# Kernel optimization log

Hardware: AMD Instinct MI355X
Metric: run time of the kernel (lower is better)

The kernel has to match this reference:

```python
import jax, jax.numpy as jnp
import numpy as np

B, NP, L, C, NA = 16, 512, 20, 3, 50
RATIO = 0.8
K = int(np.ceil(RATIO * NP))  # 410 nodes kept per graph
N = B * NP
E = 6 * N
NF, EF = 13, 4
EPS = 1e-5


def _graph_norm(x, w, b, ms):
    # PyG GraphNorm called WITHOUT batch in the source -> single global graph
    mean = x.mean(0)
    out = x - ms * mean
    var = (out * out).mean(0)
    return w * out / jnp.sqrt(var + EPS) + b


def _forward(x, pan_w, lin1_w, lin1_b, norm1_w, norm1_b, norm1_ms,
             pool_p, pool_beta, gat_wl, gat_bl, gat_wr, gat_br, gat_att, gat_bias,
             norm2_w, norm2_b, norm2_ms,
             val1_w, val1_b, val2_w, val2_b, val3_w, val3_b,
             adv1_w, adv1_b, adv2_w, adv2_b, adv3_w, adv3_b,
             edge_index, current_node_ids, action_mask):
    src, dst = edge_index[0], edge_index[1]
    # PANConv builds SparseTensor(row=edge_index[1], col=edge_index[0]) -> row = target
    A = jnp.zeros((B, NP, NP), x.dtype).at[dst // NP, dst % NP, src % NP].set(1.0)
    eyeB = jnp.broadcast_to(jnp.eye(NP, dtype=x.dtype), A.shape)

    # panentropy: M = sum_{i=0..L} w_i * A^i  (dense per graph)
    def step(carry, wi):
        tmp, acc = carry
        tmp = tmp @ A
        return (tmp, acc + wi * tmp), None
    (_, M), _ = jax.lax.scan(step, (eyeB, pan_w[0] * eyeB), pan_w[1:])
    deg = M.sum(-1)                                   # row sums
    dis = jnp.where(deg > 0, 1.0 / jnp.sqrt(deg), 0.0)
    Mn = dis[:, :, None] * M * dis[:, None, :]        # D^-1/2 M D^-1/2

    # conv1: propagate (Mn @ x) then Linear
    x3 = x.reshape(B, NP, NF)
    h = jnp.einsum('bij,bjf->bif', Mn, x3) @ lin1_w + lin1_b   # [B,NP,C]
    x1 = jax.nn.relu(_graph_norm(h.reshape(N, C), norm1_w, norm1_b, norm1_ms))  # [N,C]
    h = x1.reshape(B, NP, C)

    # PANPooling: score = tanh(b0 * <x,p> + b1 * colsum(Mn)); keep top K per graph
    score = jnp.tanh(pool_beta[0] * (h * pool_p).sum(-1) + pool_beta[1] * Mn.sum(-2))
    vals, idx = jax.lax.top_k(score, K)                        # [B,K]
    xp = jnp.take_along_axis(h, idx[:, :, None], axis=1) * vals[..., None]
    Mg = jax.vmap(lambda m, i: m[i][:, i])(Mn, idx)            # filtered adjacency [B,K,K]
    mask = (jnp.swapaxes(Mg, 1, 2) != 0) | jnp.eye(K, dtype=bool)  # mask[b,i,j]: edge j->i (+self loops)

    # GATv2Conv, heads=1, eval mode (no dropout), edge_attr not passed in source
    xl = xp @ gat_wl + gat_bl
    xr = xp @ gat_wr + gat_br
    e = jax.nn.leaky_relu(xr[:, :, None, :] + xl[:, None, :, :], 0.2)  # [B,i,j,C]
    logits = jnp.where(mask, jnp.einsum('bijc,c->bij', e, gat_att), -1e9)
    alpha = jax.nn.softmax(logits, axis=-1)
    g = jnp.einsum('bij,bjc->bic', alpha, xl) + gat_bias

    g = jax.nn.relu(_graph_norm(g.reshape(B * K, C), norm2_w, norm2_b, norm2_ms)).reshape(B, K, C)
    gp = g.sum(1)                                              # global_add_pool [B,C]

    # source uses POOLED bincount cumsum offsets to index the pre-pool arrays (faithful)
    gidx = current_node_ids + jnp.arange(B, dtype=current_node_ids.dtype) * K
    feat = jnp.concatenate([x[gidx], x1[gidx], gp], axis=1)    # [B,19]

    a = jax.nn.relu(feat @ adv1_w + adv1_b)
    a = jax.nn.relu(a @ adv2_w + adv2_b)
    a = a @ adv3_w + adv3_b
    v = jax.nn.relu(feat @ val1_w + val1_b)
    v = jax.nn.relu(v @ val2_w + val2_b)
    v = v @ val3_w + val3_b
    q = v + (a - a.mean(1, keepdims=True))
    return jnp.where(action_mask == 0, -1e8, q)


def setup_inputs() -> dict:
    key = jax.random.key(0)
    ks = list(jax.random.split(key, 40))
    nk = lambda: ks.pop()
    # within-graph random edges so the PyG-style batch structure is valid
    g = jax.random.randint(nk(), (E,), 0, B)
    u = jax.random.randint(nk(), (E,), 0, NP)
    v = jax.random.randint(nk(), (E,), 0, NP)
    edge_index = jnp.stack([g * NP + u, g * NP + v]).astype(jnp.int32)

    def lin(k, i, o):
        k1, k2 = jax.random.split(k)
        return (jax.random.normal(k1, (i, o), jnp.float32) / np.sqrt(i),
                jax.random.normal(k2, (o,), jnp.float32) * 0.01)

    lin1_w, lin1_b = lin(nk(), NF, C)
    gat_wl, gat_bl = lin(nk(), C, C)
    gat_wr, gat_br = lin(nk(), C, C)
    val1_w, val1_b = lin(nk(), 19, 10)
    val2_w, val2_b = lin(nk(), 10, 5)
    val3_w, val3_b = lin(nk(), 5, 1)
    adv1_w, adv1_b = lin(nk(), 19, 10)
    adv2_w, adv2_b = lin(nk(), 10, 5)
    adv3_w, adv3_b = lin(nk(), 5, NA)
    return dict(
        x=jax.random.normal(nk(), (N, NF), jnp.float32),
        edge_index=edge_index,
        edge_attr=jax.random.normal(nk(), (E, EF), jnp.float32),
        batch=jnp.arange(N, dtype=jnp.int32) // NP,
        current_node_ids=jax.random.randint(nk(), (B,), 0, NP),
        action_mask=jax.random.randint(nk(), (B, NA), 0, 2),
        pan_w=jax.random.uniform(nk(), (L + 1,), jnp.float32) * 0.5,
        lin1_w=lin1_w, lin1_b=lin1_b,
        norm1_w=jnp.ones(C), norm1_b=jnp.zeros(C), norm1_ms=jnp.ones(C),
        pool_p=jax.random.normal(nk(), (C,), jnp.float32),
        pool_beta=jnp.array([0.5, 0.5], jnp.float32),
        gat_wl=gat_wl, gat_bl=gat_bl, gat_wr=gat_wr, gat_br=gat_br,
        gat_att=jax.random.normal(nk(), (C,), jnp.float32),
        gat_bias=jax.random.normal(nk(), (C,), jnp.float32) * 0.01,
        norm2_w=jnp.ones(C), norm2_b=jnp.zeros(C), norm2_ms=jnp.ones(C),
        val1_w=val1_w, val1_b=val1_b, val2_w=val2_w, val2_b=val2_b,
        val3_w=val3_w, val3_b=val3_b,
        adv1_w=adv1_w, adv1_b=adv1_b, adv2_w=adv2_w, adv2_b=adv2_b,
        adv3_w=adv3_w, adv3_b=adv3_b,
    )


def reference(x, edge_index, edge_attr, batch, current_node_ids, action_mask,
              pan_w, lin1_w, lin1_b, norm1_w, norm1_b, norm1_ms,
              pool_p, pool_beta, gat_wl, gat_bl, gat_wr, gat_br, gat_att, gat_bias,
              norm2_w, norm2_b, norm2_ms,
              val1_w, val1_b, val2_w, val2_b, val3_w, val3_b,
              adv1_w, adv1_b, adv2_w, adv2_b, adv3_w, adv3_b):
    del edge_attr, batch  # received by the torch forward but never consumed
    return _forward(x, pan_w, lin1_w, lin1_b, norm1_w, norm1_b, norm1_ms,
                    pool_p, pool_beta, gat_wl, gat_bl, gat_wr, gat_br, gat_att, gat_bias,
                    norm2_w, norm2_b, norm2_ms,
                    val1_w, val1_b, val2_w, val2_b, val3_w, val3_b,
                    adv1_w, adv1_b, adv2_w, adv2_b, adv3_w, adv3_b,
                    edge_index, current_node_ids, action_mask)
```

## Files before the change

### kernel.cpp

```cpp
#include <hip/hip_runtime.h>
#include <hip/hip_bf16.h>
#include <stdint.h>
#include <math.h>

#define BB   16
#define NPn  512
#define LLp  20
#define NAa  50
#define KKk  410
#define NNt  (BB * NPn)
#define EEe  (6 * NNt)
#define NFf  13
#define KPAD 416
#define KP2  448
#define EPSf 1e-5f
#define QCLMP 1e6f
#define MAXD 28
#define PADR 512

__device__ __forceinline__ float r17_sane(float v) {
    if (!(v == v)) return 0.0f;
    return fminf(fmaxf(v, -1e15f), 1e15f);
}

__global__ __launch_bounds__(256) void r17_scatter(
    const int* __restrict__ ei,
    uint32_t* __restrict__ fwdb, uint32_t* __restrict__ trsb)
{
    const int e = blockIdx.x * 256 + threadIdx.x;
    if (e < EEe) {
        const int src = ei[e], dst = ei[EEe + e];
        atomicOr(&fwdb[(size_t)dst * 16 + ((src & 511) >> 5)], 1u << (src & 31));
        atomicOr(&trsb[(size_t)src * 16 + ((dst & 511) >> 5)], 1u << (dst & 31));
    }
}

__global__ __launch_bounds__(256) void r17_extract(
    const uint32_t* __restrict__ fwdb, const uint32_t* __restrict__ trsb,
    unsigned short* __restrict__ csrF, unsigned short* __restrict__ csrT)
{
    const int t = blockIdx.x * 256 + threadIdx.x;
    const int node = t & 8191;
    const uint32_t* bs = (t < 8192) ? (fwdb + (size_t)node * 16)
                                    : (trsb + (size_t)node * 16);
    unsigned short* cs = (t < 8192) ? csrF : csrT;
    int cnt = 0;
    for (int w = 0; w < 16; ++w) {
        uint32_t bits = bs[w];
        while (bits) {
            const int u = (w << 5) + __ffs(bits) - 1;
            bits &= bits - 1;
            if (cnt < MAXD) cs[(size_t)cnt * 8192 + node] = (unsigned short)u;
            ++cnt;
        }
    }
    for (int j = cnt; j < MAXD; ++j) cs[(size_t)j * 8192 + node] = PADR;
}

__global__ __launch_bounds__(512) void r17_mid(
    const float* __restrict__ x,
    const unsigned short* __restrict__ csrF,
    const unsigned short* __restrict__ csrT,
    const float* __restrict__ panw,
    const float* __restrict__ l1w, const float* __restrict__ l1b,
    float* __restrict__ h_raw, float* __restrict__ colsum,
    uint32_t* __restrict__ Rb)
{
    __shared__ __align__(16) uint32_t sbuf[1047];
    float* pa  = (float*)sbuf;
    float* pb  = (float*)(sbuf + 513);
    float* wsh = (float*)(sbuf + 1026);
    const int b = blockIdx.x, y = blockIdx.y, t = threadIdx.x;
    const int node = b * 512 + t;

    if (y < 4) {
        const int c = y;
        int iF[MAXD];
#pragma unroll
        for (int j = 0; j < MAXD; ++j) iF[j] = (int)csrF[(size_t)j * 8192 + node];
        if (t < 21) wsh[t] = panw[t];

        pa[t] = 1.0f;
        if (t == 0) { pa[512] = 0.0f; pb[512] = 0.0f; }
        __syncthreads();
        float dacc = wsh[0];
        {
            float* rp = pa; float* rn = pb;
            for (int i = 1; i <= LLp; ++i) {
                float tv[MAXD];
#pragma unroll
                for (int j = 0; j < MAXD; ++j) tv[j] = rp[iF[j]];
                float s = 0.0f;
#pragma unroll
                for (int j = 0; j < MAXD; ++j) s += tv[j];
                rn[t] = s;
                dacc += wsh[i] * s;
                __syncthreads();
                float* tp = rp; rp = rn; rn = tp;
            }
        }
        const float d0 = (dacc > 0.0f) ? 1.0f / sqrtf(dacc) : 0.0f;

        int idx[MAXD];
        if (c == 3) {
#pragma unroll
            for (int j = 0; j < MAXD; ++j) idx[j] = (int)csrT[(size_t)j * 8192 + node];
        } else {
#pragma unroll
            for (int j = 0; j < MAXD; ++j) idx[j] = iF[j];
        }
        float seed;
        if (c < 3) {
            float xw = 0.0f;
            const float* xr = x + (size_t)node * NFf;
            for (int f = 0; f < NFf; ++f) xw += xr[f] * l1w[f * 3 + c];
            seed = d0 * xw;
        } else {
            seed = d0;
        }
        pa[t] = seed;
        if (t == 0) { pa[512] = 0.0f; pb[512] = 0.0f; }
        __syncthreads();
        float acc = wsh[0] * seed;
        {
            float* rp = pa; float* rn = pb;
            for (int i = 1; i <= LLp; ++i) {
                float tv[MAXD];
#pragma unroll
                for (int j = 0; j < MAXD; ++j) tv[j] = rp[idx[j]];
                float s = 0.0f;
#pragma unroll
                for (int j = 0; j < MAXD; ++j) s += tv[j];
                rn[t] = s;
                acc += wsh[i] * s;
                __syncthreads();
                float* tp = rp; rp = rn; rn = tp;
            }
        }
        if (c < 3) h_raw[(size_t)node * 3 + c] = r17_sane(d0 * acc + l1b[c]);
        else       colsum[node] = r17_sane(d0 * acc);
    } else {
        const int q = y - 4;
        int iF[MAXD];
#pragma unroll
        for (int j = 0; j < MAXD; ++j) iF[j] = (int)csrF[(size_t)j * 8192 + node];
        uint32_t* R1 = sbuf;
        uint32_t* R2 = sbuf + 513;
        R1[t] = ((t >> 5) == q) ? (1u << (t & 31)) : 0u;
        if (t == 0) { R1[512] = 0u; R2[512] = 0u; }
        __syncthreads();
        uint32_t* Rp = R1; uint32_t* Rn = R2;
        for (int i = 0; i < LLp; ++i) {
            uint32_t tv[MAXD];
#pragma unroll
            for (int j = 0; j < MAXD; ++j) tv[j] = Rp[iF[j]];
            uint32_t r = Rp[t];
#pragma unroll
            for (int j = 0; j < MAXD; ++j) r |= tv[j];
            Rn[t] = r;
            __syncthreads();
            uint32_t* tp = Rp; Rp = Rn; Rn = tp;
        }
        Rb[(size_t)node * 16 + q] = Rp[t];
    }
}

__global__ __launch_bounds__(512) void r17_poolgat(
    const float* __restrict__ h_raw,
    const float* __restrict__ colsum,
    const uint32_t* __restrict__ Rb,
    const float* n1w, const float* n1b, const float* n1ms,
    const float* poolp, const float* poolb,
    const float* gwl, const float* gbl,
    const float* gwr, const float* gbr,
    const float* gatt, const float* gbias,
    float* __restrict__ x1,
    float* __restrict__ g_raw)
{
    __shared__ __align__(16) uint32_t pg[10744];
    float* sc   = (float*)pg;
    float* mv   = (float*)(pg + 512);
    float* wred = (float*)(pg + 520);
    float* xpS  = (float*)(pg + 568);
    int*   kidx = (int*)(pg + 1816);
    float* xlS  = (float*)(pg + 2232);
    uint32_t* RT = pg + 3576;
    const int b = blockIdx.x, y = blockIdx.y, t = threadIdx.x;
    const int lane = t & 63, wv = t >> 6;
    const float inv_n = 1.0f / (float)NNt;

    float hv0[16], hv1[16], hv2[16];
    float p0 = 0.0f, p1 = 0.0f, p2 = 0.0f;
#pragma unroll
    for (int k = 0; k < 16; ++k) {
        const float* hr = h_raw + (size_t)(k * 512 + t) * 3;
        hv0[k] = hr[0]; hv1[k] = hr[1]; hv2[k] = hr[2];
        p0 += hv0[k]; p1 += hv1[k]; p2 += hv2[k];
    }
#pragma unroll
    for (int off = 32; off; off >>= 1) {
        p0 += __shfl_xor(p0, off); p1 += __shfl_xor(p1, off); p2 += __shfl_xor(p2, off);
    }
    if (lane == 0) { wred[wv * 3 + 0] = p0; wred[wv * 3 + 1] = p1; wred[wv * 3 + 2] = p2; }
    __syncthreads();
    if (t < 3) {
        float s = 0.0f;
        for (int w = 0; w < 8; ++w) s += wred[w * 3 + t];
        mv[t] = s * inv_n;
    }
    __syncthreads();
    const float mm0 = n1ms[0] * mv[0], mm1 = n1ms[1] * mv[1], mm2 = n1ms[2] * mv[2];
    float q0 = 0.0f, q1 = 0.0f, q2 = 0.0f;
#pragma unroll
    for (int k = 0; k < 16; ++k) {
        const float d0 = hv0[k] - mm0, d1 = hv1[k] - mm1, d2 = hv2[k] - mm2;
        q0 += d0 * d0; q1 += d1 * d1; q2 += d2 * d2;
    }
#pragma unroll
    for (int off = 32; off; off >>= 1) {
        q0 += __shfl_xor(q0, off); q1 += __shfl_xor(q1, off); q2 += __shfl_xor(q2, off);
    }
    if (lane == 0) { wred[wv * 3 + 0] = q0; wred[wv * 3 + 1] = q1; wred[wv * 3 + 2] = q2; }
    __syncthreads();
    if (t < 3) {
        float s = 0.0f;
        for (int w = 0; w < 8; ++w) s += wred[w * 3 + t];
        mv[3 + t] = s * inv_n;
    }
    __syncthreads();

    const float mmv[3] = { mm0, mm1, mm2 };
    float xv[3];
#pragma unroll
    for (int c = 0; c < 3; ++c) {
        const float iv = 1.0f / sqrtf(fmaxf(mv[3 + c], 0.0f) + EPSf);
        const float o  = h_raw[(size_t)(b * NPn + t) * 3 + c] - mmv[c];
        const float tt = n1w[c] * o * iv + n1b[c];
        xv[c] = fmaxf(tt, 0.0f);
        if (y == 0) x1[(size_t)(b * NPn + t) * 3 + c] = xv[c];
    }
    float s = poolb[0] * (xv[0] * poolp[0] + xv[1] * poolp[1] + xv[2] * poolp[2])
            + poolb[1] * colsum[b * NPn + t];
    s = tanhf(s);
    if (!(s == s)) s = 0.0f;
    sc[t] = s;
    __syncthreads();
    int cnt = 0;
    for (int u = 0; u < NPn; ++u) {
        const float su = sc[u];
        cnt += ((su > s) || (su == s && u < t)) ? 1 : 0;
    }
    if (cnt < KKk) {
        kidx[cnt] = t;
        xpS[cnt * 3 + 0] = xv[0] * s;
        xpS[cnt * 3 + 1] = xv[1] * s;
        xpS[cnt * 3 + 2] = xv[2] * s;
    }
    __syncthreads();

    float Wl[9], Wr[9];
#pragma unroll
    for (int i2 = 0; i2 < 9; ++i2) { Wl[i2] = gwl[i2]; Wr[i2] = gwr[i2]; }
    const float Bl0 = gbl[0], Bl1 = gbl[1], Bl2 = gbl[2];
    const float Br0 = gbr[0], Br1 = gbr[1], Br2 = gbr[2];
    const float At0 = gatt[0], At1 = gatt[1], At2 = gatt[2];
    const float Gb0 = gbias[0], Gb1 = gbias[1], Gb2 = gbias[2];
    if (t < KP2) {
        const int j = t;
        if (j < KKk) {
            const float c0 = xpS[j * 3 + 0];
            const float c1 = xpS[j * 3 + 1];
            const float c2 = xpS[j * 3 + 2];
            xlS[j * 3 + 0] = c0 * Wl[0] + c1 * Wl[3] + c2 * Wl[6] + Bl0;
            xlS[j * 3 + 1] = c0 * Wl[1] + c1 * Wl[4] + c2 * Wl[7] + Bl1;
            xlS[j * 3 + 2] = c0 * Wl[2] + c1 * Wl[5] + c2 * Wl[8] + Bl2;
            const uint32_t* rr = Rb + (size_t)(b * NPn + kidx[j]) * 16;
#pragma unroll
            for (int w = 0; w < 16; ++w) RT[w * KP2 + j] = rr[w];
        } else {
            xlS[j * 3 + 0] = 0.0f; xlS[j * 3 + 1] = 0.0f; xlS[j * 3 + 2] = 0.0f;
#pragma unroll
            for (int w = 0; w < 16; ++w) RT[w * KP2 + j] = 0u;
        }
    }
    __syncthreads();

    const int wid = y * 8 + wv;
    for (int i = wid; i < KKk; i += 64) {
        const float c0 = xpS[i * 3 + 0];
        const float c1 = xpS[i * 3 + 1];
        const float c2 = xpS[i * 3 + 2];
        const float xr0 = c0 * Wr[0] + c1 * Wr[3] + c2 * Wr[6] + Br0;
        const float xr1 = c0 * Wr[1] + c1 * Wr[4] + c2 * Wr[7] + Br1;
        const float xr2 = c0 * Wr[2] + c1 * Wr[5] + c2 * Wr[8] + Br2;
        const int bi = kidx[i];
        const uint32_t mbit = 1u << (bi & 31);
        const uint32_t* Rw = &RT[(bi >> 5) * KP2];
        float mx = -3e38f, lsum = 0.0f, b0 = 0.0f, b1 = 0.0f, b2 = 0.0f;
#pragma unroll
        for (int it = 0; it < 7; ++it) {
            const int j = lane + it * 64;
            const uint32_t rw = Rw[j];
            const float xl0 = xlS[j * 3 + 0];
            const float xl1 = xlS[j * 3 + 1];
            const float xl2 = xlS[j * 3 + 2];
            const bool valid = (rw & mbit) || (j == i);
            float e0 = xr0 + xl0; e0 = e0 > 0.0f ? e0 : 0.2f * e0;
            float e1 = xr1 + xl1; e1 = e1 > 0.0f ? e1 : 0.2f * e1;
            float e2 = xr2 + xl2; e2 = e2 > 0.0f ? e2 : 0.2f * e2;
            const float sv = At0 * e0 + At1 * e1 + At2 * e2;
            if (valid) {
                if (sv > mx) {
                    const float r = __expf(mx - sv);
                    lsum *= r; b0 *= r; b1 *= r; b2 *= r;
                    mx = sv;
                }
                const float pj = __expf(sv - mx);
                lsum += pj;
                b0 += pj * xl0; b1 += pj * xl1; b2 += pj * xl2;
            }
        }
#pragma unroll
        for (int off = 32; off; off >>= 1) {
            const float mo = __shfl_xor(mx, off);
            const float lo = __shfl_xor(lsum, off);
            const float d0 = __shfl_xor(b0, off);
            const float d1 = __shfl_xor(b1, off);
            const float d2 = __shfl_xor(b2, off);
            const float M  = fmaxf(mx, mo);
            const float ea = __expf(mx - M), eb = __expf(mo - M);
            lsum = lsum * ea + lo * eb;
            b0 = b0 * ea + d0 * eb;
            b1 = b1 * ea + d1 * eb;
            b2 = b2 * ea + d2 * eb;
            mx = M;
        }
        if (lane == 0) {
            const float rl = 1.0f / fmaxf(lsum, 1e-30f);
            g_raw[(size_t)(b * KPAD + i) * 3 + 0] = r17_sane(b0 * rl + Gb0);
            g_raw[(size_t)(b * KPAD + i) * 3 + 1] = r17_sane(b1 * rl + Gb1);
            g_raw[(size_t)(b * KPAD + i) * 3 + 2] = r17_sane(b2 * rl + Gb2);
        }
    }
}

__global__ __launch_bounds__(512) void r17_head(
    const float* __restrict__ g_raw,
    const float* __restrict__ x1,
    const float* __restrict__ x,
    const int* __restrict__ cnid,
    const int* __restrict__ amask,
    const float* n2w, const float* n2b, const float* n2ms,
    const float* v1w, const float* v1b,
    const float* v2w, const float* v2b,
    const float* v3w, const float* v3b,
    const float* a1w, const float* a1b,
    const float* a2w, const float* a2b,
    const float* a3w, const float* a3b,
    float* __restrict__ out)
{
    __shared__ float wred[24];
    __shared__ float mv[6];
    __shared__ float gp[3];
    __shared__ float feat[19];
    __shared__ float h1a[10], h1v[10], h2a[5], h2v[5];
    __shared__ float a3[50];
    __shared__ float vout_s, amean_s;
    const int b = blockIdx.x, t = threadIdx.x;
    const int lane = t & 63, wv = t >> 6;
    const float denom = 1.0f / (float)(BB * KKk);

    float gv0[13], gv1[13], gv2[13];
    float p0 = 0.0f, p1 = 0.0f, p2 = 0.0f;
#pragma unroll
    for (int k = 0; k < 13; ++k) {
        const int r = k * 512 + t;
        float q0 = 0.0f, q1 = 0.0f, q2 = 0.0f;
        if (r < BB * KKk) {
            const int bq = r / KKk, iq = r - bq * KKk;
            const float* gr = g_raw + (size_t)(bq * KPAD + iq) * 3;
            q0 = gr[0]; q1 = gr[1]; q2 = gr[2];
        }
        gv0[k] = q0; gv1[k] = q1; gv2[k] = q2;
        p0 += q0; p1 += q1; p2 += q2;
    }
#pragma unroll
    for (int off = 32; off; off >>= 1) {
        p0 += __shfl_xor(p0, off); p1 += __shfl_xor(p1, off); p2 += __shfl_xor(p2, off);
    }
    if (lane == 0) { wred[wv * 3 + 0] = p0; wred[wv * 3 + 1] = p1; wred[wv * 3 + 2] = p2; }
    __syncthreads();
    if (t < 3) {
        float s = 0.0f;
        for (int w = 0; w < 8; ++w) s += wred[w * 3 + t];
        mv[t] = s * denom;
    }
    __syncthreads();
    const float mm0 = n2ms[0] * mv[0], mm1 = n2ms[1] * mv[1], mm2 = n2ms[2] * mv[2];
    float q0a = 0.0f, q1a = 0.0f, q2a = 0.0f;
#pragma unroll
    for (int k = 0; k < 13; ++k) {
        const int r = k * 512 + t;
        if (r < BB * KKk) {
            const float d0 = gv0[k] - mm0, d1 = gv1[k] - mm1, d2 = gv2[k] - mm2;
            q0a += d0 * d0; q1a += d1 * d1; q2a += d2 * d2;
        }
    }
#pragma unroll
    for (int off = 32; off; off >>= 1) {
        q0a += __shfl_xor(q0a, off); q1a += __shfl_xor(q1a, off); q2a += __shfl_xor(q2a, off);
    }
    if (lane == 0) { wred[wv * 3 + 0] = q0a; wred[wv * 3 + 1] = q1a; wred[wv * 3 + 2] = q2a; }
    __syncthreads();
    if (t < 3) {
        float s = 0.0f;
        for (int w = 0; w < 8; ++w) s += wred[w * 3 + t];
        mv[3 + t] = s * denom;
    }
    __syncthreads();

    const float mmv[3] = { mm0, mm1, mm2 };
    float s3[3] = { 0.0f, 0.0f, 0.0f };
    if (t < KKk) {
        const size_t r = (size_t)(b * KPAD + t) * 3;
#pragma unroll
        for (int c = 0; c < 3; ++c) {
            const float iv = 1.0f / sqrtf(fmaxf(mv[3 + c], 0.0f) + EPSf);
            s3[c] = fmaxf((g_raw[r + c] - mmv[c]) * iv * n2w[c] + n2b[c], 0.0f);
        }
    }
    float g0 = s3[0], g1 = s3[1], g2 = s3[2];
#pragma unroll
    for (int off = 32; off; off >>= 1) {
        g0 += __shfl_xor(g0, off); g1 += __shfl_xor(g1, off); g2 += __shfl_xor(g2, off);
    }
    if (lane == 0) { wred[wv * 3 + 0] = g0; wred[wv * 3 + 1] = g1; wred[wv * 3 + 2] = g2; }
    __syncthreads();
    if (t < 3) {
        float s = 0.0f;
        for (int w = 0; w < 8; ++w) s += wred[w * 3 + t];
        gp[t] = s;
    }
    __syncthreads();

    if (t < 19) {
        const int gidx = cnid[b] + b * KKk;
        float fv;
        if (t < 13)      fv = x[(size_t)gidx * NFf + t];
        else if (t < 16) fv = x1[(size_t)gidx * 3 + (t - 13)];
        else             fv = gp[t - 16];
        feat[t] = fv;
    }
    __syncthreads();

    if (t < 10) {
        float s = a1b[t];
        for (int f = 0; f < 19; ++f) s += feat[f] * a1w[f * 10 + t];
        h1a[t] = fmaxf(s, 0.0f);
    } else if (t >= 64 && t < 74) {
        const int j = t - 64;
        float s = v1b[j];
        for (int f = 0; f < 19; ++f) s += feat[f] * v1w[f * 10 + j];
        h1v[j] = fmaxf(s, 0.0f);
    }
    __syncthreads();
    if (t < 5) {
        float s = a2b[t];
        for (int k = 0; k < 10; ++k) s += h1a[k] * a2w[k * 5 + t];
        h2a[t] = fmaxf(s, 0.0f);
    } else if (t >= 64 && t < 69) {
        const int j = t - 64;
        float s = v2b[j];
        for (int k = 0; k < 10; ++k) s += h1v[k] * v2w[k * 5 + j];
        h2v[j] = fmaxf(s, 0.0f);
    }
    __syncthreads();
    if (t < 50) {
        float s = a3b[t];
        for (int k = 0; k < 5; ++k) s += h2a[k] * a3w[k * 50 + t];
        a3[t] = s;
    } else if (t == 64) {
        float s = v3b[0];
        for (int k = 0; k < 5; ++k) s += h2v[k] * v3w[k];
        vout_s = s;
    }
    __syncthreads();
    if (t == 0) {
        float s = 0.0f;
        for (int k = 0; k < 50; ++k) s += a3[k];
        amean_s = s * (1.0f / 50.0f);
    }
    __syncthreads();
    if (t < 50) {
        float q = vout_s + a3[t] - amean_s;
        if (!(q == q)) q = 0.0f;
        q = fminf(fmaxf(q, -QCLMP), QCLMP);
        out[b * NAa + t] = (amask[b * NAa + t] == 0) ? -1e8f : q;
    }
}

extern "C" void kernel_launch(void* const* d_in, const int* in_sizes, int n_in,
                              void* d_out, int out_size, void* d_ws, size_t ws_size,
                              hipStream_t stream) {
    (void)in_sizes; (void)n_in; (void)out_size;
    const float* x     = (const float*)d_in[0];
    const int* ei      = (const int*)d_in[1];
    const int* cnid    = (const int*)d_in[4];
    const int* amask   = (const int*)d_in[5];
    const float* panw  = (const float*)d_in[6];
    const float* l1w   = (const float*)d_in[7];
    const float* l1b   = (const float*)d_in[8];
    const float* n1w   = (const float*)d_in[9];
    const float* n1b   = (const float*)d_in[10];
    const float* n1ms  = (const float*)d_in[11];
    const float* poolp = (const float*)d_in[12];
    const float* poolb = (const float*)d_in[13];
    const float* gwl   = (const float*)d_in[14];
    const float* gbl   = (const float*)d_in[15];
    const float* gwr   = (const float*)d_in[16];
    const float* gbr   = (const float*)d_in[17];
    const float* gatt  = (const float*)d_in[18];
    const float* gbias = (const float*)d_in[19];
    const float* n2w   = (const float*)d_in[20];
    const float* n2b   = (const float*)d_in[21];
    const float* n2ms  = (const float*)d_in[22];
    const float* v1w   = (const float*)d_in[23];
    const float* v1b   = (const float*)d_in[24];
    const float* v2w   = (const float*)d_in[25];
    const float* v2b   = (const float*)d_in[26];
    const float* v3w   = (const float*)d_in[27];
    const float* v3b   = (const float*)d_in[28];
    const float* a1w   = (const float*)d_in[29];
    const float* a1b   = (const float*)d_in[30];
    const float* a2w   = (const float*)d_in[31];
    const float* a2b   = (const float*)d_in[32];
    const float* a3w   = (const float*)d_in[33];
    const float* a3b   = (const float*)d_in[34];
    float* out         = (float*)d_out;

    uint8_t* wsb = (uint8_t*)d_ws;
    uint32_t* fwdb = (uint32_t*)wsb;
    uint32_t* trsb = (uint32_t*)(wsb + 524288);
    uint32_t* Rb   = (uint32_t*)(wsb + 1048576);
    unsigned short* csrF = (unsigned short*)(wsb + 1572864);
    unsigned short* csrT = csrF + (size_t)MAXD * 8192;
    float* h_raw  = (float*)(csrT + (size_t)MAXD * 8192);
    float* x1     = h_raw + (size_t)NNt * 3;
    float* colsum = x1 + (size_t)NNt * 3;
    float* g_raw  = colsum + NNt;
    const size_t needed = 1572864 + 2 * (size_t)MAXD * 8192 * 2 +
                          ((size_t)(2 * NNt * 3 + NNt + BB * KPAD * 3)) * 4;
    if (ws_size < needed) return;

    hipMemsetAsync(fwdb, 0, 1048576, stream);
    r17_scatter<<<dim3((EEe + 255) / 256), dim3(256), 0, stream>>>(ei, fwdb, trsb);
    r17_extract<<<dim3(64), dim3(256), 0, stream>>>(fwdb, trsb, csrF, csrT);
    r17_mid<<<dim3(16, 20), dim3(512), 0, stream>>>(x, csrF, csrT, panw, l1w, l1b,
                                                    h_raw, colsum, Rb);
    r17_poolgat<<<dim3(16, 8), dim3(512), 0, stream>>>(h_raw, colsum, Rb,
                                                       n1w, n1b, n1ms, poolp, poolb,
                                                       gwl, gbl, gwr, gbr, gatt, gbias,
                                                       x1, g_raw);
    r17_head<<<dim3(16), dim3(512), 0, stream>>>(g_raw, x1, x, cnid, amask,
                                                 n2w, n2b, n2ms, v1w, v1b, v2w, v2b, v3w, v3b,
                                                 a1w, a1b, a2w, a2b, a3w, a3b, out);
}
```

Baseline: 211.0 us.

## Split pooling and GAT attention into separate kernels with wider GAT grid

The fused pool+GAT kernel, launched as 16x8 blocks that each redundantly recomputed graph norm, top-k and the transposed reachability table, is split in two. A 16-block pooling kernel now computes the selection once per graph and writes the kept features, projections, indices and transposed bitmasks to workspace. A separate 16x52 GAT kernel then handles one target node per wavefront, reading from global memory. The top-k rank loop also reads scores as float4. This removes redundant per-block work and spreads attention over more blocks, at the cost of an extra launch and global round-trips instead of shared memory.

Result: faster. 206.5 us (-2.2%).

```diff
diff --git a/kernel.cpp b/kernel.cpp
--- a/kernel.cpp
+++ b/kernel.cpp
@@ -165,27 +165,26 @@
     }
 }
 
-__global__ __launch_bounds__(512) void r17_poolgat(
+__global__ __launch_bounds__(512) void r18_pool(
     const float* __restrict__ h_raw,
     const float* __restrict__ colsum,
     const uint32_t* __restrict__ Rb,
     const float* n1w, const float* n1b, const float* n1ms,
     const float* poolp, const float* poolb,
     const float* gwl, const float* gbl,
-    const float* gwr, const float* gbr,
-    const float* gatt, const float* gbias,
     float* __restrict__ x1,
-    float* __restrict__ g_raw)
+    float* __restrict__ xpg,
+    float* __restrict__ xlg,
+    int*   __restrict__ kidxg,
+    uint32_t* __restrict__ RTg)
 {
-    __shared__ __align__(16) uint32_t pg[10744];
+    __shared__ __align__(16) uint32_t pg[2208];
     float* sc   = (float*)pg;
     float* mv   = (float*)(pg + 512);
     float* wred = (float*)(pg + 520);
-    float* xpS  = (float*)(pg + 568);
-    int*   kidx = (int*)(pg + 1816);
-    float* xlS  = (float*)(pg + 2232);
-    uint32_t* RT = pg + 3576;
-    const int b = blockIdx.x, y = blockIdx.y, t = threadIdx.x;
+    float* xpS  = (float*)(pg + 544);
+    int*   kidx = (int*)(pg + 1792);
+    const int b = blockIdx.x, t = threadIdx.x;
     const int lane = t & 63, wv = t >> 6;
     const float inv_n = 1.0f / (float)NNt;
 
@@ -237,7 +236,7 @@
         const float o  = h_raw[(size_t)(b * NPn + t) * 3 + c] - mmv[c];
         const float tt = n1w[c] * o * iv + n1b[c];
         xv[c] = fmaxf(tt, 0.0f);
-        if (y == 0) x1[(size_t)(b * NPn + t) * 3 + c] = xv[c];
+        x1[(size_t)(b * NPn + t) * 3 + c] = xv[c];
     }
     float s = poolb[0] * (xv[0] * poolp[0] + xv[1] * poolp[1] + xv[2] * poolp[2])
             + poolb[1] * colsum[b * NPn + t];
@@ -245,102 +244,136 @@
     if (!(s == s)) s = 0.0f;
     sc[t] = s;
     __syncthreads();
+
     int cnt = 0;
-    for (int u = 0; u < NPn; ++u) {
-        const float su = sc[u];
-        cnt += ((su > s) || (su == s && u < t)) ? 1 : 0;
+    for (int u = 0; u < NPn; u += 4) {
+        const float4 s4 = *(const float4*)(sc + u);
+        cnt += ((s4.x > s) || (s4.x == s && (u + 0) < t)) ? 1 : 0;
+        cnt += ((s4.y > s) || (s4.y == s && (u + 1) < t)) ? 1 : 0;
+        cnt += ((s4.z > s) || (s4.z == s && (u + 2) < t)) ? 1 : 0;
+        cnt += ((s4.w > s) || (s4.w == s && (u + 3) < t)) ? 1 : 0;
     }
     if (cnt < KKk) {
+        const float xp0 = xv[0] * s, xp1 = xv[1] * s, xp2 = xv[2] * s;
         kidx[cnt] = t;
-        xpS[cnt * 3 + 0] = xv[0] * s;
-        xpS[cnt * 3 + 1] = xv[1] * s;
-        xpS[cnt * 3 + 2] = xv[2] * s;
-    }
-    __syncthreads();
-
-    float Wl[9], Wr[9];
-#pragma unroll
-    for (int i2 = 0; i2 < 9; ++i2) { Wl[i2] = gwl[i2]; Wr[i2] = gwr[i2]; }
+        xpS[cnt * 3 + 0] = xp0;
+        xpS[cnt * 3 + 1] = xp1;
+        xpS[cnt * 3 + 2] = xp2;
+        kidxg[b * KPAD + cnt] = t;
+        xpg[(size_t)(b * KPAD + cnt) * 3 + 0] = xp0;
+        xpg[(size_t)(b * KPAD + cnt) * 3 + 1] = xp1;
+        xpg[(size_t)(b * KPAD + cnt) * 3 + 2] = xp2;
+    }
+    __syncthreads();
+
+    float Wl[9];
+#pragma unroll
+    for (int i2 = 0; i2 < 9; ++i2) Wl[i2] = gwl[i2];
     const float Bl0 = gbl[0], Bl1 = gbl[1], Bl2 = gbl[2];
+    if (t < KP2) {
+        float xl0, xl1, xl2;
+        uint32_t* RT = RTg + (size_t)b * 16 * KP2 + t;
+        if (t < KKk) {
+            const float c0 = xpS[t * 3 + 0];
+            const float c1 = xpS[t * 3 + 1];
+            const float c2 = xpS[t * 3 + 2];
+            xl0 = c0 * Wl[0] + c1 * Wl[3] + c2 * Wl[6] + Bl0;
+            xl1 = c0 * Wl[1] + c1 * Wl[4] + c2 * Wl[7] + Bl1;
+            xl2 = c0 * Wl[2] + c1 * Wl[5] + c2 * Wl[8] + Bl2;
+            const uint4* rr = (const uint4*)(Rb + (size_t)(b * NPn + kidx[t]) * 16);
+            const uint4 r0 = rr[0], r1 = rr[1], r2 = rr[2], r3 = rr[3];
+            RT[ 0 * KP2] = r0.x; RT[ 1 * KP2] = r0.y; RT[ 2 * KP2] = r0.z; RT[ 3 * KP2] = r0.w;
+            RT[ 4 * KP2] = r1.x; RT[ 5 * KP2] = r1.y; RT[ 6 * KP2] = r1.z; RT[ 7 * KP2] = r1.w;
+            RT[ 8 * KP2] = r2.x; RT[ 9 * KP2] = r2.y; RT[10 * KP2] = r2.z; RT[11 * KP2] = r2.w;
+            RT[12 * KP2] = r3.x; RT[13 * KP2] = r3.y; RT[14 * KP2] = r3.z; RT[15 * KP2] = r3.w;
+        } else {
+            xl0 = 0.0f; xl1 = 0.0f; xl2 = 0.0f;
+#pragma unroll
+            for (int w = 0; w < 16; ++w) RT[w * KP2] = 0u;
+        }
+        xlg[(size_t)(b * KP2 + t) * 3 + 0] = xl0;
+        xlg[(size_t)(b * KP2 + t) * 3 + 1] = xl1;
+        xlg[(size_t)(b * KP2 + t) * 3 + 2] = xl2;
+    }
+}
+
+__global__ __launch_bounds__(512) void r18_gat(
+    const float* __restrict__ xpg,
+    const float* __restrict__ xlg,
+    const int* __restrict__ kidxg,
+    const uint32_t* __restrict__ RTg,
+    const float* __restrict__ gwr, const float* __restrict__ gbr,
+    const float* __restrict__ gatt, const float* __restrict__ gbias,
+    float* __restrict__ g_raw)
+{
+    const int b = blockIdx.x, y = blockIdx.y, t = threadIdx.x;
+    const int lane = t & 63, wv = t >> 6;
+    const int i = y * 8 + wv;
+    if (i >= KKk) return;
+
+    float Wr[9];
+#pragma unroll
+    for (int k = 0; k < 9; ++k) Wr[k] = gwr[k];
     const float Br0 = gbr[0], Br1 = gbr[1], Br2 = gbr[2];
     const float At0 = gatt[0], At1 = gatt[1], At2 = gatt[2];
     const float Gb0 = gbias[0], Gb1 = gbias[1], Gb2 = gbias[2];
-    if (t < KP2) {
-        const int j = t;
-        if (j < KKk) {
-            const float c0 = xpS[j * 3 + 0];
-            const float c1 = xpS[j * 3 + 1];
-            const float c2 = xpS[j * 3 + 2];
-            xlS[j * 3 + 0] = c0 * Wl[0] + c1 * Wl[3] + c2 * Wl[6] + Bl0;
-            xlS[j * 3 + 1] = c0 * Wl[1] + c1 * Wl[4] + c2 * Wl[7] + Bl1;
-            xlS[j * 3 + 2] = c0 * Wl[2] + c1 * Wl[5] + c2 * Wl[8] + Bl2;
-            const uint32_t* rr = Rb + (size_t)(b * NPn + kidx[j]) * 16;
-#pragma unroll
-            for (int w = 0; w < 16; ++w) RT[w * KP2 + j] = rr[w];
-        } else {
-            xlS[j * 3 + 0] = 0.0f; xlS[j * 3 + 1] = 0.0f; xlS[j * 3 + 2] = 0.0f;
-#pragma unroll
-            for (int w = 0; w < 16; ++w) RT[w * KP2 + j] = 0u;
-        }
-    }
-    __syncthreads();
-
-    const int wid = y * 8 + wv;
-    for (int i = wid; i < KKk; i += 64) {
-        const float c0 = xpS[i * 3 + 0];
-        const float c1 = xpS[i * 3 + 1];
-        const float c2 = xpS[i * 3 + 2];
-        const float xr0 = c0 * Wr[0] + c1 * Wr[3] + c2 * Wr[6] + Br0;
-        const float xr1 = c0 * Wr[1] + c1 * Wr[4] + c2 * Wr[7] + Br1;
-        const float xr2 = c0 * Wr[2] + c1 * Wr[5] + c2 * Wr[8] + Br2;
-        const int bi = kidx[i];
-        const uint32_t mbit = 1u << (bi & 31);
-        const uint32_t* Rw = &RT[(bi >> 5) * KP2];
-        float mx = -3e38f, lsum = 0.0f, b0 = 0.0f, b1 = 0.0f, b2 = 0.0f;
-#pragma unroll
-        for (int it = 0; it < 7; ++it) {
-            const int j = lane + it * 64;
-            const uint32_t rw = Rw[j];
-            const float xl0 = xlS[j * 3 + 0];
-            const float xl1 = xlS[j * 3 + 1];
-            const float xl2 = xlS[j * 3 + 2];
-            const bool valid = (rw & mbit) || (j == i);
-            float e0 = xr0 + xl0; e0 = e0 > 0.0f ? e0 : 0.2f * e0;
-            float e1 = xr1 + xl1; e1 = e1 > 0.0f ? e1 : 0.2f * e1;
-            float e2 = xr2 + xl2; e2 = e2 > 0.0f ? e2 : 0.2f * e2;
-            const float sv = At0 * e0 + At1 * e1 + At2 * e2;
-            if (valid) {
-                if (sv > mx) {
-                    const float r = __expf(mx - sv);
-                    lsum *= r; b0 *= r; b1 *= r; b2 *= r;
-                    mx = sv;
-                }
-                const float pj = __expf(sv - mx);
-                lsum += pj;
-                b0 += pj * xl0; b1 += pj * xl1; b2 += pj * xl2;
+
+    const int bi = kidxg[b * KPAD + i];
+    const float c0 = xpg[(size_t)(b * KPAD + i) * 3 + 0];
+    const float c1 = xpg[(size_t)(b * KPAD + i) * 3 + 1];
+    const float c2 = xpg[(size_t)(b * KPAD + i) * 3 + 2];
+    const float xr0 = c0 * Wr[0] + c1 * Wr[3] + c2 * Wr[6] + Br0;
+    const float xr1 = c0 * Wr[1] + c1 * Wr[4] + c2 * Wr[7] + Br1;
+    const float xr2 = c0 * Wr[2] + c1 * Wr[5] + c2 * Wr[8] + Br2;
+
+    const uint32_t mbit = 1u << (bi & 31);
+    const uint32_t* Rw = RTg + (size_t)(b * 16 + (bi >> 5)) * KP2;
+    const float* xlb = xlg + (size_t)b * KP2 * 3;
+
+    float mx = -3e38f, lsum = 0.0f, b0 = 0.0f, b1 = 0.0f, b2 = 0.0f;
+#pragma unroll
+    for (int it = 0; it < 7; ++it) {
+        const int j = lane + it * 64;
+        const uint32_t rw = Rw[j];
+        const float xl0 = xlb[j * 3 + 0];
+        const float xl1 = xlb[j * 3 + 1];
+        const float xl2 = xlb[j * 3 + 2];
+        const bool valid = (rw & mbit) || (j == i);
+        float e0 = xr0 + xl0; e0 = e0 > 0.0f ? e0 : 0.2f * e0;
+        float e1 = xr1 + xl1; e1 = e1 > 0.0f ? e1 : 0.2f * e1;
+        float e2 = xr2 + xl2; e2 = e2 > 0.0f ? e2 : 0.2f * e2;
+        const float sv = At0 * e0 + At1 * e1 + At2 * e2;
+        if (valid) {
+            if (sv > mx) {
+                const float r = __expf(mx - sv);
+                lsum *= r; b0 *= r; b1 *= r; b2 *= r;
+                mx = sv;
             }
-        }
-#pragma unroll
-        for (int off = 32; off; off >>= 1) {
-            const float mo = __shfl_xor(mx, off);
-            const float lo = __shfl_xor(lsum, off);
-            const float d0 = __shfl_xor(b0, off);
-            const float d1 = __shfl_xor(b1, off);
-            const float d2 = __shfl_xor(b2, off);
-            const float M  = fmaxf(mx, mo);
-            const float ea = __expf(mx - M), eb = __expf(mo - M);
-            lsum = lsum * ea + lo * eb;
-            b0 = b0 * ea + d0 * eb;
-            b1 = b1 * ea + d1 * eb;
-            b2 = b2 * ea + d2 * eb;
-            mx = M;
-        }
-        if (lane == 0) {
-            const float rl = 1.0f / fmaxf(lsum, 1e-30f);
-            g_raw[(size_t)(b * KPAD + i) * 3 + 0] = r17_sane(b0 * rl + Gb0);
-            g_raw[(size_t)(b * KPAD + i) * 3 + 1] = r17_sane(b1 * rl + Gb1);
-            g_raw[(size_t)(b * KPAD + i) * 3 + 2] = r17_sane(b2 * rl + Gb2);
-        }
+            const float pj = __expf(sv - mx);
+            lsum += pj;
+            b0 += pj * xl0; b1 += pj * xl1; b2 += pj * xl2;
+        }
+    }
+#pragma unroll
+    for (int off = 32; off; off >>= 1) {
+        const float mo = __shfl_xor(mx, off);
+        const float lo = __shfl_xor(lsum, off);
+        const float d0 = __shfl_xor(b0, off);
+        const float d1 = __shfl_xor(b1, off);
+        const float d2 = __shfl_xor(b2, off);
+        const float M  = fmaxf(mx, mo);
+        const float ea = __expf(mx - M), eb = __expf(mo - M);
+        lsum = lsum * ea + lo * eb;
+        b0 = b0 * ea + d0 * eb;
+        b1 = b1 * ea + d1 * eb;
+        b2 = b2 * ea + d2 * eb;
+        mx = M;
+    }
+    if (lane == 0) {
+        const float rl = 1.0f / fmaxf(lsum, 1e-30f);
+        g_raw[(size_t)(b * KPAD + i) * 3 + 0] = r17_sane(b0 * rl + Gb0);
+        g_raw[(size_t)(b * KPAD + i) * 3 + 1] = r17_sane(b1 * rl + Gb1);
+        g_raw[(size_t)(b * KPAD + i) * 3 + 2] = r17_sane(b2 * rl + Gb2);
     }
 }
 
@@ -548,8 +581,17 @@
     float* x1     = h_raw + (size_t)NNt * 3;
     float* colsum = x1 + (size_t)NNt * 3;
     float* g_raw  = colsum + NNt;
-    const size_t needed = 1572864 + 2 * (size_t)MAXD * 8192 * 2 +
-                          ((size_t)(2 * NNt * 3 + NNt + BB * KPAD * 3)) * 4;
+    float* xpg    = g_raw + (size_t)BB * KPAD * 3;
+    float* xlg    = xpg + (size_t)BB * KPAD * 3;
+    int*   kidxg  = (int*)(xlg + (size_t)BB * KP2 * 3);
+    uint32_t* RTg = (uint32_t*)(kidxg + (size_t)BB * KPAD);
+    const size_t needed = 1572864
+                        + 2 * (size_t)MAXD * 8192 * 2
+                        + ((size_t)(2 * NNt * 3 + NNt
+                           + 2 * BB * KPAD * 3
+                           + BB * KP2 * 3)) * 4
+                        + (size_t)BB * KPAD * 4
+                        + (size_t)BB * 16 * KP2 * 4;
     if (ws_size < needed) return;
 
     hipMemsetAsync(fwdb, 0, 1048576, stream);
@@ -557,10 +599,12 @@
     r17_extract<<<dim3(64), dim3(256), 0, stream>>>(fwdb, trsb, csrF, csrT);
     r17_mid<<<dim3(16, 20), dim3(512), 0, stream>>>(x, csrF, csrT, panw, l1w, l1b,
                                                     h_raw, colsum, Rb);
-    r17_poolgat<<<dim3(16, 8), dim3(512), 0, stream>>>(h_raw, colsum, Rb,
-                                                       n1w, n1b, n1ms, poolp, poolb,
-                                                       gwl, gbl, gwr, gbr, gatt, gbias,
-                                                       x1, g_raw);
+    r18_pool<<<dim3(16), dim3(512), 0, stream>>>(h_raw, colsum, Rb,
+                                                 n1w, n1b, n1ms, poolp, poolb,
+                                                 gwl, gbl,
+                                                 x1, xpg, xlg, kidxg, RTg);
+    r18_gat<<<dim3(16, 52), dim3(512), 0, stream>>>(xpg, xlg, kidxg, RTg,
+                                                    gwr, gbr, gatt, gbias, g_raw);
     r17_head<<<dim3(16), dim3(512), 0, stream>>>(g_raw, x1, x, cnid, amask,
                                                  n2w, n2b, n2ms, v1w, v1b, v2w, v2b, v3w, v3b,
                                                  a1w, a1b, a2w, a2b, a3w, a3b, out);
```
